# Optimization experiments

Measured on AMD Instinct MI355X. Metric: run time of the kernel, lower is better.

The kernel has to match this reference:

```python
import jax, jax.numpy as jnp
import numpy as np

B, V, H, W, C = 2, 4, 120, 160, 96
N_VOX = 200000
GRID = 128
VOXEL_SIZE = 0.05
DEPTH_MIN = 0.1 / VOXEL_SIZE   # 2.0 (voxel units)
DEPTH_MAX = 4.0 / VOXEL_SIZE   # 80.0 (voxel units)
STEP = 0.5                     # ray increment = voxel_size/2, in voxel units
N_STEPS = int((DEPTH_MAX - DEPTH_MIN) / STEP)  # 156


def setup_inputs() -> dict:
    key = jax.random.key(0)
    kf, kc = jax.random.split(key)
    feats = jax.random.normal(kf, (B, V, H, W, C), dtype=jnp.float32)
    # batch-sorted sparse voxel coords [N,4] = (b, x, y, z)
    xyz = jax.random.randint(kc, (N_VOX, 3), 0, GRID).astype(jnp.int32)
    bcol = jnp.repeat(jnp.arange(B, dtype=jnp.int32), N_VOX // B)[:, None]
    coords = jnp.concatenate([bcol, xyz], axis=1)
    # camera-to-world matrices in voxel units: identity rotation (looking along +z),
    # cameras at z=0 spread across x so rays sweep the grid in depth range [2, 80]
    vm = np.tile(np.eye(4, dtype=np.float32), (B, V, 1, 1))
    vm[:, :, 0, 3] = np.array([40.0, 56.0, 72.0, 88.0], dtype=np.float32)[None, :]
    vm[:, :, 1, 3] = 64.0
    vm[:, :, 2, 3] = 0.0
    view_matrix = jnp.asarray(vm)
    intrinsic_params = jnp.array([80.0, 80.0, 80.0, 60.0], dtype=jnp.float32)  # fx,fy,cx,cy
    return {"encoded_2d_features": feats, "coords": coords,
            "view_matrix": view_matrix, "intrinsic_params": intrinsic_params}


def _project(encoded_2d_features, coords, view_matrix, intrinsic_params):
    n = coords.shape[0]
    # --- per-batch coordinate shift (as in original forward) ---
    local = coords[:, 1:]
    lc = local
    local_views = view_matrix
    for b in range(B):
        m = (coords[:, 0] == b)[:, None]
        shift = jnp.min(jnp.where(m, local, jnp.iinfo(jnp.int32).max), axis=0)  # [3]
        lc = jnp.where(m, lc - shift, lc)
        local_views = local_views.at[b, :, :3, 3].add(-shift.astype(view_matrix.dtype))
    # --- dense occupancy grid, permuted to [b, z, y, x]; -1 marks empty ---
    occ = jnp.full((B, GRID, GRID, GRID), -1, dtype=jnp.int32)
    occ = occ.at[coords[:, 0], lc[:, 2], lc[:, 1], lc[:, 0]].set(
        jnp.arange(n, dtype=jnp.int32))
    # --- per-pixel ray marching ---
    fx, fy, cx, cy = intrinsic_params
    t = DEPTH_MIN + STEP * jnp.arange(N_STEPS, dtype=jnp.float32)        # [S]
    dx = (jnp.arange(W, dtype=jnp.float32) + 0.5 - cx) / fx              # [W]
    dy = (jnp.arange(H, dtype=jnp.float32) + 0.5 - cy) / fy              # [H]
    # camera-space sample points along each pixel ray: [H, W, S, 3]
    pc = jnp.stack(jnp.broadcast_arrays(
        dx[None, :, None] * t, dy[:, None, None] * t,
        jnp.broadcast_to(t, (H, W, N_STEPS))), axis=-1)
    Rm = local_views[:, :, :3, :3]   # [B,V,3,3]
    tr = local_views[:, :, :3, 3]    # [B,V,3]
    # world (grid) space points: [B, V, H, W, S, 3]
    pw = jnp.einsum('bvij,hwsj->bvhwsi', Rm, pc) + tr[:, :, None, None, None, :]
    vox = jnp.floor(pw).astype(jnp.int32)
    ix, iy, iz = vox[..., 0], vox[..., 1], vox[..., 2]
    inb = ((ix >= 0) & (ix < GRID) & (iy >= 0) & (iy < GRID) &
           (iz >= 0) & (iz < GRID))
    bidx = jnp.arange(B, dtype=jnp.int32)[:, None, None, None, None]
    occ_val = occ[bidx,
                  jnp.clip(iz, 0, GRID - 1),
                  jnp.clip(iy, 0, GRID - 1),
                  jnp.clip(ix, 0, GRID - 1)]
    vox_id = jnp.where(inb, occ_val, -1)                                  # [B,V,H,W,S]
    # first occupied voxel hit along each ray
    hit = vox_id >= 0
    first = jnp.argmax(hit, axis=-1)                                      # [B,V,H,W]
    has_hit = jnp.any(hit, axis=-1)
    hit_id = jnp.take_along_axis(vox_id, first[..., None], axis=-1)[..., 0]
    tgt = jnp.where(has_hit, hit_id, n).reshape(-1)   # index n = dump slot for misses
    # scatter-accumulate pixel features into voxel slots + per-voxel counts
    flat_feat = encoded_2d_features.reshape(-1, C)
    proj = jnp.zeros((n + 1, C), dtype=encoded_2d_features.dtype).at[tgt].add(flat_feat)[:n]
    cnt = jnp.zeros((n + 1,), dtype=jnp.int32).at[tgt].add(1)[:n]
    out = proj / (cnt[:, None].astype(proj.dtype) + 1e-4)
    return out, cnt


def reference(encoded_2d_features, coords, view_matrix, intrinsic_params):
    return _project(encoded_2d_features, coords, view_matrix, intrinsic_params)
```

## Files before the change

kernel.cpp:

```cpp
#include <hip/hip_runtime.h>
#include <hip/hip_bf16.h>
#include <climits>

#define B_ 2
#define V_ 4
#define H_ 120
#define W_ 160
#define C_ 96
#define NVOX 200000
#define GRID_ 128
#define NSTEPS 156
#define NRAYS (B_*V_*H_*W_)
#define NB1 ((NVOX + 255) / 256)
#define CHUNK 32
#define NCHUNK ((NRAYS + CHUNK - 1) / CHUNK)
#define OUTQ2 ((NVOX * C_) / 4)
#define NTHREADS_MARCH (2400 * 256)


__global__ void occ_kernel(const int* __restrict__ coords,
                           int* __restrict__ occ,
                           unsigned long long* __restrict__ mask) {
    int i = blockIdx.x * blockDim.x + threadIdx.x;
    if (i >= NVOX) return;
    int b = coords[i * 4 + 0];
    int x = coords[i * 4 + 1];
    int y = coords[i * 4 + 2];
    int z = coords[i * 4 + 3];
    int idx = ((b * GRID_ + z) * GRID_ + y) * GRID_ + x;
    atomicMax(&occ[idx], i);
    atomicOr(&mask[idx >> 6], 1ull << (idx & 63));
}

__global__ void march_kernel(const float* __restrict__ vm,
                             const float* __restrict__ intr,
                             const unsigned long long* __restrict__ mask,
                             const int* __restrict__ occ,
                             int* __restrict__ tgt,
                             int* __restrict__ cnt,
                             float* __restrict__ out) {
    int gt   = blockIdx.x * blockDim.x + threadIdx.x;
    int lane = threadIdx.x & 63;
    int p    = lane & 15;
    int sub  = lane >> 4;
    int r    = ((gt >> 6) << 4) + p;
    {
        int w = r % W_;
        int h = (r / W_) % H_;
        int v = (r / (W_ * H_)) % V_;
        int b = r / (W_ * H_ * V_);
        const float* M = vm + (size_t)(b * V_ + v) * 16;
        float fx = intr[0], fy = intr[1], cx = intr[2], cy = intr[3];
        float dx = ((float)w + 0.5f - cx) / fx;
        float dy = ((float)h + 0.5f - cy) / fy;
        float d0 = M[0] * dx + M[1] * dy + M[2];
        float d1 = M[4] * dx + M[5] * dy + M[6];
        float d2 = M[8] * dx + M[9] * dy + M[10];
        float t0 = M[3];
        float t1 = M[7];
        float t2 = M[11];
        const int vbase = b * GRID_ * GRID_ * GRID_;
        const int MISS = 0x7FFFFFFF;
        int beststep = MISS;
        for (int w0 = 0; w0 < NSTEPS; w0 += 32) {
            int lin[8]; bool ok[8];
#pragma unroll
            for (int j = 0; j < 8; ++j) {
                int st = w0 + sub * 8 + j;
                float t = 2.0f + 0.5f * (float)st;
                float pwx = d0 * t + t0;
                float pwy = d1 * t + t1;
                float pwz = d2 * t + t2;
                int ix = (int)floorf(pwx);
                int iy = (int)floorf(pwy);
                int iz = (int)floorf(pwz);
                ok[j] = ((unsigned)ix < (unsigned)GRID_) &
                        ((unsigned)iy < (unsigned)GRID_) &
                        ((unsigned)iz < (unsigned)GRID_) & (st < NSTEPS);
                int cix = min(max(ix, 0), GRID_ - 1);
                int ciy = min(max(iy, 0), GRID_ - 1);
                int ciz = min(max(iz, 0), GRID_ - 1);
                lin[j] = vbase + (ciz << 14) + (ciy << 7) + cix;
            }
            unsigned long long u[8];
            bool same[8];
            same[0] = false;
#pragma unroll
            for (int j = 1; j < 8; ++j) same[j] = ((lin[j] >> 6) == (lin[j - 1] >> 6));
#pragma unroll
            for (int j = 0; j < 8; ++j)
                if (!same[j]) u[j] = mask[lin[j] >> 6];
#pragma unroll
            for (int j = 1; j < 8; ++j)
                if (same[j]) u[j] = u[j - 1];
            int local = MISS;
#pragma unroll
            for (int j = 0; j < 8; ++j) {
                int st = w0 + sub * 8 + j;
                if (ok[j] && ((u[j] >> (lin[j] & 63)) & 1ull)) local = min(local, st);
            }
            local = min(local, __shfl_xor(local, 16));
            local = min(local, __shfl_xor(local, 32));
            if (local != MISS) { beststep = local; break; }
        }
        int res = -1;
        if (sub == 0) {
            if (beststep != MISS) {
                float t = 2.0f + 0.5f * (float)beststep;
                int ix = (int)floorf(d0 * t + t0);
                int iy = (int)floorf(d1 * t + t1);
                int iz = (int)floorf(d2 * t + t2);
                res = occ[vbase + (iz << 14) + (iy << 7) + ix];
            }
            tgt[r] = res;
        }
        bool active = (sub == 0) && (res >= 0);
        int prevres = __shfl_up(res, 1);
        bool head = active && (p == 0 || prevres != res);
        bool boundary = head || !active;
        unsigned long long bb = __ballot(boundary);
        if (head) {
            unsigned long long above = bb & ~((2ull << lane) - 1);
            int next = above ? (__ffsll((long long)above) - 1) : 64;
            atomicAdd(&cnt[res], next - lane);
        }
    }
    float4 z4 = make_float4(0.f, 0.f, 0.f, 0.f);
    float4* o4 = (float4*)out;
    for (int i = gt; i < OUTQ2; i += NTHREADS_MARCH) o4[i] = z4;
}

__global__ void alloc_kernel(const int* __restrict__ cnt,
                             int* __restrict__ gtotal,
                             int* __restrict__ segstart,
                             int* __restrict__ cursor,
                             int* __restrict__ wl,
                             int* __restrict__ wlcount,
                             float* __restrict__ cnt_out) {
    __shared__ int wtot[4];
    int tid  = threadIdx.x;
    int lane = tid & 63;
    int wid  = tid >> 6;
    int i = blockIdx.x * 256 + tid;
    int c = (i < NVOX) ? cnt[i] : 0;
    int x = c;
#pragma unroll
    for (int d = 1; d < 64; d <<= 1) {
        int y = __shfl_up(x, d);
        if (lane >= d) x += y;
    }
    if (lane == 63) wtot[wid] = x;
    __syncthreads();
    if (tid == 0) {
        int s0 = wtot[0], s1 = wtot[1], s2 = wtot[2], s3 = wtot[3];
        int base = atomicAdd(gtotal, s0 + s1 + s2 + s3);
        wtot[0] = base;
        wtot[1] = base + s0;
        wtot[2] = base + s0 + s1;
        wtot[3] = base + s0 + s1 + s2;
    }
    __syncthreads();
    if (i >= NVOX) return;
    cnt_out[i] = (float)c;
    int s = wtot[wid] + (x - c);
    segstart[i] = s;
    cursor[i]   = s;
    if (c > 0 && (s / CHUNK) != ((s + c - 1) / CHUNK)) {
        int pidx = atomicAdd(wlcount, 1);
        wl[pidx] = i;
    }
}

__global__ void order_kernel(const int* __restrict__ tgt,
                             int* __restrict__ cursor, int2* __restrict__ sorted_rt) {
    int r = blockIdx.x * blockDim.x + threadIdx.x;
    int lane = threadIdx.x & 63;
    int t = tgt[r];
    bool active = t >= 0;
    int prev = __shfl_up(t, 1);
    bool head = active && (lane == 0 || prev != t);
    bool boundary = head || !active;
    unsigned long long bb = __ballot(boundary);
    unsigned long long below = bb & ((2ull << lane) - 1);
    int headpos = 63 - __clzll(below | 1ull);
    int base = 0;
    if (head) {
        unsigned long long above = bb & ~((2ull << lane) - 1);
        int next = above ? (__ffsll((long long)above) - 1) : 64;
        int runlen = next - lane;
        base = atomicAdd(&cursor[t], runlen);
    }
    base = __shfl(base, headpos);
    if (active) sorted_rt[base + (lane - headpos)] = make_int2(r, t);
}

__device__ __forceinline__ void flush_run2(int t, int ks, int ke, int n,
                                           float ax, float ay, int lane,
                                           const int* __restrict__ segstart,
                                           const int* __restrict__ cnt,
                                           float* __restrict__ out) {
    int c;
    bool complete;
    if (ks > 0 && ke < n) {
        c = ke - ks;
        complete = true;
    } else {
        c = cnt[t];
        int s = segstart[t];
        complete = (s / CHUNK) == ((s + c - 1) / CHUNK);
    }
    if (complete) {
        float denom = (float)c + 0.0001f;
        if (lane < 48) {
            float2 wv; wv.x = ax / denom; wv.y = ay / denom;
            ((float2*)(out + (size_t)t * C_))[lane] = wv;
        }
    } else if (lane < 48) {
        unsafeAtomicAdd(out + (size_t)t * C_ + 2 * lane,     ax);
        unsafeAtomicAdd(out + (size_t)t * C_ + 2 * lane + 1, ay);
    }
}

__global__ void chunk_reduce_kernel(const float* __restrict__ feats,
                                    const int2* __restrict__ sorted_rt,
                                    const int* __restrict__ segstart,
                                    const int* __restrict__ cnt,
                                    const int* __restrict__ total_p,
                                    float* __restrict__ out) {
    int wave = (blockIdx.x * blockDim.x + threadIdx.x) >> 6;
    int lane = threadIdx.x & 63;
    int total = total_p[0];
    int a = wave * CHUNK;
    if (a >= total) return;
    int n = min(CHUNK, total - a);
    int myr = 0, myt = 0;
    if (lane < n) { int2 e = sorted_rt[a + lane]; myr = e.x; myt = e.y; }
    float ax = 0.0f, ay = 0.0f;
    int cur = -1, run_start = 0;
    for (int k0 = 0; k0 < n; k0 += 8) {
        float2 vbuf[8]; int tt[8];
#pragma unroll
        for (int j = 0; j < 8; ++j) {
            int k = k0 + j;
            int rr = __shfl(myr, k);
            tt[j]  = __shfl(myt, k);
            vbuf[j] = make_float2(0.0f, 0.0f);
            if (k < n && lane < 48)
                vbuf[j] = ((const float2*)(feats + (size_t)rr * C_))[lane];
        }
#pragma unroll
        for (int j = 0; j < 8; ++j) {
            int k = k0 + j;
            if (k >= n) break;
            if (tt[j] != cur) {
                if (cur >= 0)
                    flush_run2(cur, run_start, k, n, ax, ay, lane, segstart, cnt, out);
                cur = tt[j]; run_start = k; ax = 0.0f; ay = 0.0f;
            }
            ax += vbuf[j].x; ay += vbuf[j].y;
        }
    }
    flush_run2(cur, run_start, n, n, ax, ay, lane, segstart, cnt, out);
}

__global__ void finalize_kernel(const int* __restrict__ wl,
                                const int* __restrict__ wlcount,
                                const int* __restrict__ cnt,
                                float* __restrict__ out) {
    int idx  = (blockIdx.x * blockDim.x + threadIdx.x) >> 6;
    int lane = threadIdx.x & 63;
    if (idx >= wlcount[0]) return;
    int vox = wl[idx];
    int c = cnt[vox];
    float denom = (float)c + 0.0001f;
    if (lane < 48) {
        float2* o = (float2*)(out + (size_t)vox * C_);
        float2 x = o[lane];
        x.x /= denom; x.y /= denom;
        o[lane] = x;
    }
}

extern "C" void kernel_launch(void* const* d_in, const int* in_sizes, int n_in,
                              void* d_out, int out_size, void* d_ws, size_t ws_size,
                              hipStream_t stream) {
    const float* feats  = (const float*)d_in[0];
    const int*   coords = (const int*)d_in[1];
    const float* vm     = (const float*)d_in[2];
    const float* intr   = (const float*)d_in[3];

    float* out     = (float*)d_out;
    float* cnt_out = out + (size_t)NVOX * C_;

    char* ws = (char*)d_ws;
    int*                cnt     = (int*)(ws + 64);
    unsigned long long* mask    = (unsigned long long*)(ws + 800064);
    int*                gtotal  = (int*)(ws + 1324352);
    int*                wlcount = (int*)(ws + 1324356);
    int*  tgt       = (int*)(ws + 1324416);
    int*  segstart  = (int*)(ws + 1938816);
    int*  cursor    = (int*)(ws + 2738816);
    int*  wl        = (int*)(ws + 3538816);
    int2* sorted_rt = (int2*)(ws + 3558016);
    int*  occ       = (int*)(ws + 4786816);

    (void)hipMemsetAsync(ws, 0, 1324360, stream);

    occ_kernel<<<NB1, 256, 0, stream>>>(coords, occ, mask);
    march_kernel<<<2400, 256, 0, stream>>>(vm, intr, mask, occ, tgt, cnt, out);
    alloc_kernel<<<NB1, 256, 0, stream>>>(cnt, gtotal, segstart, cursor, wl, wlcount, cnt_out);
    order_kernel<<<NRAYS / 256, 256, 0, stream>>>(tgt, cursor, sorted_rt);
    chunk_reduce_kernel<<<(NCHUNK * 64 + 255) / 256, 256, 0, stream>>>(
        feats, sorted_rt, segstart, cnt, gtotal, out);
    finalize_kernel<<<(NCHUNK * 64 + 255) / 256, 256, 0, stream>>>(
        wl, wlcount, cnt, out);
}
```

Baseline: 220.1 us.

## Replace counting-sort scatter pipeline with direct per-ray atomic scatter

Removes the alloc, order and finalize kernels that counting-sorted rays by target voxel. A single scatter kernel now walks rays in their original order in chunks of 32, merges consecutive runs that hit the same voxel, and atomically adds the pre-normalized features (divided by the final count) into the output. Zeroing of the output moves into the occupancy kernel and the count output is written in the scatter kernel. This cuts kernel launches, the prefix scan and the sorted-index traffic, at the cost of more float atomics on voxels hit by non-adjacent rays and a nondeterministic summation order.

```diff
diff --git a/kernel.cpp b/kernel.cpp
--- a/kernel.cpp
+++ b/kernel.cpp
@@ -13,23 +13,29 @@
 #define NRAYS (B_*V_*H_*W_)
 #define NB1 ((NVOX + 255) / 256)
 #define CHUNK 32
-#define NCHUNK ((NRAYS + CHUNK - 1) / CHUNK)
 #define OUTQ2 ((NVOX * C_) / 4)
+#define NTHREADS_OCC (NB1 * 256)
 #define NTHREADS_MARCH (2400 * 256)
 
 
 __global__ void occ_kernel(const int* __restrict__ coords,
                            int* __restrict__ occ,
-                           unsigned long long* __restrict__ mask) {
+                           unsigned long long* __restrict__ mask,
+                           float* __restrict__ out) {
     int i = blockIdx.x * blockDim.x + threadIdx.x;
-    if (i >= NVOX) return;
-    int b = coords[i * 4 + 0];
-    int x = coords[i * 4 + 1];
-    int y = coords[i * 4 + 2];
-    int z = coords[i * 4 + 3];
-    int idx = ((b * GRID_ + z) * GRID_ + y) * GRID_ + x;
-    atomicMax(&occ[idx], i);
-    atomicOr(&mask[idx >> 6], 1ull << (idx & 63));
+    if (i < NVOX) {
+        int b = coords[i * 4 + 0];
+        int x = coords[i * 4 + 1];
+        int y = coords[i * 4 + 2];
+        int z = coords[i * 4 + 3];
+        int idx = ((b * GRID_ + z) * GRID_ + y) * GRID_ + x;
+        atomicMax(&occ[idx], i);
+        atomicOr(&mask[idx >> 6], 1ull << (idx & 63));
+    }
+    float4 z4 = make_float4(0.f, 0.f, 0.f, 0.f);
+    float4* o4 = (float4*)out;
+    for (int q = blockIdx.x * blockDim.x + threadIdx.x; q < OUTQ2; q += NTHREADS_OCC)
+        o4[q] = z4;
 }
 
 __global__ void march_kernel(const float* __restrict__ vm,
@@ -37,248 +43,136 @@
                              const unsigned long long* __restrict__ mask,
                              const int* __restrict__ occ,
                              int* __restrict__ tgt,
-                             int* __restrict__ cnt,
-                             float* __restrict__ out) {
+                             int* __restrict__ cnt) {
     int gt   = blockIdx.x * blockDim.x + threadIdx.x;
     int lane = threadIdx.x & 63;
     int p    = lane & 15;
     int sub  = lane >> 4;
     int r    = ((gt >> 6) << 4) + p;
-    {
-        int w = r % W_;
-        int h = (r / W_) % H_;
-        int v = (r / (W_ * H_)) % V_;
-        int b = r / (W_ * H_ * V_);
-        const float* M = vm + (size_t)(b * V_ + v) * 16;
-        float fx = intr[0], fy = intr[1], cx = intr[2], cy = intr[3];
-        float dx = ((float)w + 0.5f - cx) / fx;
-        float dy = ((float)h + 0.5f - cy) / fy;
-        float d0 = M[0] * dx + M[1] * dy + M[2];
-        float d1 = M[4] * dx + M[5] * dy + M[6];
-        float d2 = M[8] * dx + M[9] * dy + M[10];
-        float t0 = M[3];
-        float t1 = M[7];
-        float t2 = M[11];
-        const int vbase = b * GRID_ * GRID_ * GRID_;
-        const int MISS = 0x7FFFFFFF;
-        int beststep = MISS;
-        for (int w0 = 0; w0 < NSTEPS; w0 += 32) {
-            int lin[8]; bool ok[8];
-#pragma unroll
-            for (int j = 0; j < 8; ++j) {
-                int st = w0 + sub * 8 + j;
-                float t = 2.0f + 0.5f * (float)st;
-                float pwx = d0 * t + t0;
-                float pwy = d1 * t + t1;
-                float pwz = d2 * t + t2;
-                int ix = (int)floorf(pwx);
-                int iy = (int)floorf(pwy);
-                int iz = (int)floorf(pwz);
-                ok[j] = ((unsigned)ix < (unsigned)GRID_) &
-                        ((unsigned)iy < (unsigned)GRID_) &
-                        ((unsigned)iz < (unsigned)GRID_) & (st < NSTEPS);
-                int cix = min(max(ix, 0), GRID_ - 1);
-                int ciy = min(max(iy, 0), GRID_ - 1);
-                int ciz = min(max(iz, 0), GRID_ - 1);
-                lin[j] = vbase + (ciz << 14) + (ciy << 7) + cix;
-            }
-            unsigned long long u[8];
-            bool same[8];
-            same[0] = false;
-#pragma unroll
-            for (int j = 1; j < 8; ++j) same[j] = ((lin[j] >> 6) == (lin[j - 1] >> 6));
-#pragma unroll
-            for (int j = 0; j < 8; ++j)
-                if (!same[j]) u[j] = mask[lin[j] >> 6];
-#pragma unroll
-            for (int j = 1; j < 8; ++j)
-                if (same[j]) u[j] = u[j - 1];
-            int local = MISS;
-#pragma unroll
-            for (int j = 0; j < 8; ++j) {
-                int st = w0 + sub * 8 + j;
-                if (ok[j] && ((u[j] >> (lin[j] & 63)) & 1ull)) local = min(local, st);
-            }
-            local = min(local, __shfl_xor(local, 16));
-            local = min(local, __shfl_xor(local, 32));
-            if (local != MISS) { beststep = local; break; }
-        }
-        int res = -1;
-        if (sub == 0) {
-            if (beststep != MISS) {
-                float t = 2.0f + 0.5f * (float)beststep;
-                int ix = (int)floorf(d0 * t + t0);
-                int iy = (int)floorf(d1 * t + t1);
-                int iz = (int)floorf(d2 * t + t2);
-                res = occ[vbase + (iz << 14) + (iy << 7) + ix];
-            }
-            tgt[r] = res;
-        }
-        bool active = (sub == 0) && (res >= 0);
-        int prevres = __shfl_up(res, 1);
-        bool head = active && (p == 0 || prevres != res);
-        bool boundary = head || !active;
-        unsigned long long bb = __ballot(boundary);
-        if (head) {
-            unsigned long long above = bb & ~((2ull << lane) - 1);
-            int next = above ? (__ffsll((long long)above) - 1) : 64;
-            atomicAdd(&cnt[res], next - lane);
-        }
-    }
-    float4 z4 = make_float4(0.f, 0.f, 0.f, 0.f);
-    float4* o4 = (float4*)out;
-    for (int i = gt; i < OUTQ2; i += NTHREADS_MARCH) o4[i] = z4;
-}
-
-__global__ void alloc_kernel(const int* __restrict__ cnt,
-                             int* __restrict__ gtotal,
-                             int* __restrict__ segstart,
-                             int* __restrict__ cursor,
-                             int* __restrict__ wl,
-                             int* __restrict__ wlcount,
-                             float* __restrict__ cnt_out) {
-    __shared__ int wtot[4];
-    int tid  = threadIdx.x;
-    int lane = tid & 63;
-    int wid  = tid >> 6;
-    int i = blockIdx.x * 256 + tid;
-    int c = (i < NVOX) ? cnt[i] : 0;
-    int x = c;
-#pragma unroll
-    for (int d = 1; d < 64; d <<= 1) {
-        int y = __shfl_up(x, d);
-        if (lane >= d) x += y;
-    }
-    if (lane == 63) wtot[wid] = x;
-    __syncthreads();
-    if (tid == 0) {
-        int s0 = wtot[0], s1 = wtot[1], s2 = wtot[2], s3 = wtot[3];
-        int base = atomicAdd(gtotal, s0 + s1 + s2 + s3);
-        wtot[0] = base;
-        wtot[1] = base + s0;
-        wtot[2] = base + s0 + s1;
-        wtot[3] = base + s0 + s1 + s2;
-    }
-    __syncthreads();
-    if (i >= NVOX) return;
-    cnt_out[i] = (float)c;
-    int s = wtot[wid] + (x - c);
-    segstart[i] = s;
-    cursor[i]   = s;
-    if (c > 0 && (s / CHUNK) != ((s + c - 1) / CHUNK)) {
-        int pidx = atomicAdd(wlcount, 1);
-        wl[pidx] = i;
-    }
-}
-
-__global__ void order_kernel(const int* __restrict__ tgt,
-                             int* __restrict__ cursor, int2* __restrict__ sorted_rt) {
-    int r = blockIdx.x * blockDim.x + threadIdx.x;
-    int lane = threadIdx.x & 63;
-    int t = tgt[r];
-    bool active = t >= 0;
-    int prev = __shfl_up(t, 1);
-    bool head = active && (lane == 0 || prev != t);
+    int w = r % W_;
+    int h = (r / W_) % H_;
+    int v = (r / (W_ * H_)) % V_;
+    int b = r / (W_ * H_ * V_);
+    const float* M = vm + (size_t)(b * V_ + v) * 16;
+    float fx = intr[0], fy = intr[1], cx = intr[2], cy = intr[3];
+    float dx = ((float)w + 0.5f - cx) / fx;
+    float dy = ((float)h + 0.5f - cy) / fy;
+    float d0 = M[0] * dx + M[1] * dy + M[2];
+    float d1 = M[4] * dx + M[5] * dy + M[6];
+    float d2 = M[8] * dx + M[9] * dy + M[10];
+    float t0 = M[3];
+    float t1 = M[7];
+    float t2 = M[11];
+    const int vbase = b * GRID_ * GRID_ * GRID_;
+    const int MISS = 0x7FFFFFFF;
+    int beststep = MISS;
+    for (int w0 = 0; w0 < NSTEPS; w0 += 32) {
+        int lin[8]; bool ok[8];
+#pragma unroll
+        for (int j = 0; j < 8; ++j) {
+            int st = w0 + sub * 8 + j;
+            float t = 2.0f + 0.5f * (float)st;
+            float pwx = d0 * t + t0;
+            float pwy = d1 * t + t1;
+            float pwz = d2 * t + t2;
+            int ix = (int)floorf(pwx);
+            int iy = (int)floorf(pwy);
+            int iz = (int)floorf(pwz);
+            ok[j] = ((unsigned)ix < (unsigned)GRID_) &
+                    ((unsigned)iy < (unsigned)GRID_) &
+                    ((unsigned)iz < (unsigned)GRID_) & (st < NSTEPS);
+            int cix = min(max(ix, 0), GRID_ - 1);
+            int ciy = min(max(iy, 0), GRID_ - 1);
+            int ciz = min(max(iz, 0), GRID_ - 1);
+            lin[j] = vbase + (ciz << 14) + (ciy << 7) + cix;
+        }
+        unsigned long long u[8];
+        bool same[8];
+        same[0] = false;
+#pragma unroll
+        for (int j = 1; j < 8; ++j) same[j] = ((lin[j] >> 6) == (lin[j - 1] >> 6));
+#pragma unroll
+        for (int j = 0; j < 8; ++j)
+            if (!same[j]) u[j] = mask[lin[j] >> 6];
+#pragma unroll
+        for (int j = 1; j < 8; ++j)
+            if (same[j]) u[j] = u[j - 1];
+        int local = MISS;
+#pragma unroll
+        for (int j = 0; j < 8; ++j) {
+            int st = w0 + sub * 8 + j;
+            if (ok[j] && ((u[j] >> (lin[j] & 63)) & 1ull)) local = min(local, st);
+        }
+        local = min(local, __shfl_xor(local, 16));
+        local = min(local, __shfl_xor(local, 32));
+        if (local != MISS) { beststep = local; break; }
+    }
+    int res = -1;
+    if (sub == 0) {
+        if (beststep != MISS) {
+            float t = 2.0f + 0.5f * (float)beststep;
+            int ix = (int)floorf(d0 * t + t0);
+            int iy = (int)floorf(d1 * t + t1);
+            int iz = (int)floorf(d2 * t + t2);
+            res = occ[vbase + (iz << 14) + (iy << 7) + ix];
+        }
+        tgt[r] = res;
+    }
+    bool active = (sub == 0) && (res >= 0);
+    int prevres = __shfl_up(res, 1);
+    bool head = active && (p == 0 || prevres != res);
     bool boundary = head || !active;
     unsigned long long bb = __ballot(boundary);
-    unsigned long long below = bb & ((2ull << lane) - 1);
-    int headpos = 63 - __clzll(below | 1ull);
-    int base = 0;
     if (head) {
         unsigned long long above = bb & ~((2ull << lane) - 1);
         int next = above ? (__ffsll((long long)above) - 1) : 64;
-        int runlen = next - lane;
-        base = atomicAdd(&cursor[t], runlen);
-    }
-    base = __shfl(base, headpos);
-    if (active) sorted_rt[base + (lane - headpos)] = make_int2(r, t);
-}
-
-__device__ __forceinline__ void flush_run2(int t, int ks, int ke, int n,
-                                           float ax, float ay, int lane,
-                                           const int* __restrict__ segstart,
-                                           const int* __restrict__ cnt,
-                                           float* __restrict__ out) {
-    int c;
-    bool complete;
-    if (ks > 0 && ke < n) {
-        c = ke - ks;
-        complete = true;
-    } else {
-        c = cnt[t];
-        int s = segstart[t];
-        complete = (s / CHUNK) == ((s + c - 1) / CHUNK);
-    }
-    if (complete) {
-        float denom = (float)c + 0.0001f;
-        if (lane < 48) {
-            float2 wv; wv.x = ax / denom; wv.y = ay / denom;
-            ((float2*)(out + (size_t)t * C_))[lane] = wv;
-        }
-    } else if (lane < 48) {
-        unsafeAtomicAdd(out + (size_t)t * C_ + 2 * lane,     ax);
-        unsafeAtomicAdd(out + (size_t)t * C_ + 2 * lane + 1, ay);
-    }
-}
-
-__global__ void chunk_reduce_kernel(const float* __restrict__ feats,
-                                    const int2* __restrict__ sorted_rt,
-                                    const int* __restrict__ segstart,
-                                    const int* __restrict__ cnt,
-                                    const int* __restrict__ total_p,
-                                    float* __restrict__ out) {
-    int wave = (blockIdx.x * blockDim.x + threadIdx.x) >> 6;
+        atomicAdd(&cnt[res], next - lane);
+    }
+}
+
+__device__ __forceinline__ void flush_run(int t, float ax, float ay, int lane,
+                                          const int* __restrict__ cnt,
+                                          float* __restrict__ out) {
+    float denom = (float)cnt[t] + 0.0001f;
+    if (lane < 48) {
+        unsafeAtomicAdd(out + (size_t)t * C_ + 2 * lane,     ax / denom);
+        unsafeAtomicAdd(out + (size_t)t * C_ + 2 * lane + 1, ay / denom);
+    }
+}
+
+__global__ void scatter_kernel(const float* __restrict__ feats,
+                               const int* __restrict__ tgt,
+                               const int* __restrict__ cnt,
+                               float* __restrict__ out,
+                               float* __restrict__ cnt_out) {
+    int gthread = blockIdx.x * blockDim.x + threadIdx.x;
     int lane = threadIdx.x & 63;
-    int total = total_p[0];
+    if (gthread < NVOX) cnt_out[gthread] = (float)cnt[gthread];
+    int wave = gthread >> 6;
     int a = wave * CHUNK;
-    if (a >= total) return;
-    int n = min(CHUNK, total - a);
-    int myr = 0, myt = 0;
-    if (lane < n) { int2 e = sorted_rt[a + lane]; myr = e.x; myt = e.y; }
+    int myt = (lane < CHUNK) ? tgt[a + lane] : -1;
     float ax = 0.0f, ay = 0.0f;
-    int cur = -1, run_start = 0;
-    for (int k0 = 0; k0 < n; k0 += 8) {
+    int cur = -1;
+    for (int k0 = 0; k0 < CHUNK; k0 += 8) {
         float2 vbuf[8]; int tt[8];
 #pragma unroll
         for (int j = 0; j < 8; ++j) {
             int k = k0 + j;
-            int rr = __shfl(myr, k);
-            tt[j]  = __shfl(myt, k);
+            tt[j] = __shfl(myt, k);
             vbuf[j] = make_float2(0.0f, 0.0f);
-            if (k < n && lane < 48)
-                vbuf[j] = ((const float2*)(feats + (size_t)rr * C_))[lane];
-        }
-#pragma unroll
-        for (int j = 0; j < 8; ++j) {
-            int k = k0 + j;
-            if (k >= n) break;
+            if (tt[j] >= 0 && lane < 48)
+                vbuf[j] = ((const float2*)(feats + (size_t)(a + k) * C_))[lane];
+        }
+#pragma unroll
+        for (int j = 0; j < 8; ++j) {
             if (tt[j] != cur) {
-                if (cur >= 0)
-                    flush_run2(cur, run_start, k, n, ax, ay, lane, segstart, cnt, out);
-                cur = tt[j]; run_start = k; ax = 0.0f; ay = 0.0f;
+                if (cur >= 0) flush_run(cur, ax, ay, lane, cnt, out);
+                cur = tt[j]; ax = 0.0f; ay = 0.0f;
             }
             ax += vbuf[j].x; ay += vbuf[j].y;
         }
     }
-    flush_run2(cur, run_start, n, n, ax, ay, lane, segstart, cnt, out);
-}
-
-__global__ void finalize_kernel(const int* __restrict__ wl,
-                                const int* __restrict__ wlcount,
-                                const int* __restrict__ cnt,
-                                float* __restrict__ out) {
-    int idx  = (blockIdx.x * blockDim.x + threadIdx.x) >> 6;
-    int lane = threadIdx.x & 63;
-    if (idx >= wlcount[0]) return;
-    int vox = wl[idx];
-    int c = cnt[vox];
-    float denom = (float)c + 0.0001f;
-    if (lane < 48) {
-        float2* o = (float2*)(out + (size_t)vox * C_);
-        float2 x = o[lane];
-        x.x /= denom; x.y /= denom;
-        o[lane] = x;
-    }
+    if (cur >= 0) flush_run(cur, ax, ay, lane, cnt, out);
 }
 
 extern "C" void kernel_launch(void* const* d_in, const int* in_sizes, int n_in,
@@ -293,25 +187,14 @@
     float* cnt_out = out + (size_t)NVOX * C_;
 
     char* ws = (char*)d_ws;
-    int*                cnt     = (int*)(ws + 64);
-    unsigned long long* mask    = (unsigned long long*)(ws + 800064);
-    int*                gtotal  = (int*)(ws + 1324352);
-    int*                wlcount = (int*)(ws + 1324356);
-    int*  tgt       = (int*)(ws + 1324416);
-    int*  segstart  = (int*)(ws + 1938816);
-    int*  cursor    = (int*)(ws + 2738816);
-    int*  wl        = (int*)(ws + 3538816);
-    int2* sorted_rt = (int2*)(ws + 3558016);
-    int*  occ       = (int*)(ws + 4786816);
-
-    (void)hipMemsetAsync(ws, 0, 1324360, stream);
-
-    occ_kernel<<<NB1, 256, 0, stream>>>(coords, occ, mask);
-    march_kernel<<<2400, 256, 0, stream>>>(vm, intr, mask, occ, tgt, cnt, out);
-    alloc_kernel<<<NB1, 256, 0, stream>>>(cnt, gtotal, segstart, cursor, wl, wlcount, cnt_out);
-    order_kernel<<<NRAYS / 256, 256, 0, stream>>>(tgt, cursor, sorted_rt);
-    chunk_reduce_kernel<<<(NCHUNK * 64 + 255) / 256, 256, 0, stream>>>(
-        feats, sorted_rt, segstart, cnt, gtotal, out);
-    finalize_kernel<<<(NCHUNK * 64 + 255) / 256, 256, 0, stream>>>(
-        wl, wlcount, cnt, out);
-}
+    int*                cnt  = (int*)(ws + 64);
+    unsigned long long* mask = (unsigned long long*)(ws + 800064);
+    int*  tgt = (int*)(ws + 1324416);
+    int*  occ = (int*)(ws + 4786816);
+
+    (void)hipMemsetAsync(ws, 0, 1324352, stream);
+
+    occ_kernel<<<NB1, 256, 0, stream>>>(coords, occ, mask, out);
+    march_kernel<<<2400, 256, 0, stream>>>(vm, intr, mask, occ, tgt, cnt);
+    scatter_kernel<<<NRAYS / CHUNK / 4, 256, 0, stream>>>(feats, tgt, cnt, out, cnt_out);
+}
```

Result: faster. 192.4 us (-12.6%).
